# Kernel tuning notes

Measured on AMD Instinct MI355X. Metric: run time of the kernel, lower is better.

## Reference

```python
import jax, jax.numpy as jnp
import numpy as np

ALPHA = 0.2  # LeakyReLU negative slope
NEG_INF = -9e15  # matches torch -9000000000000000.0


def setup_inputs() -> dict:
    key = jax.random.key(0)
    k1, k2, k3, k4, k5, k6 = jax.random.split(key, 6)
    N, F_in, F_out = 4096, 512, 256
    adj = jax.random.randint(k1, (N, N), 0, 2, dtype=jnp.int32)
    h = jax.random.normal(k2, (N, F_in), dtype=jnp.float32)
    # proj: Linear(F_in, F_out)
    W = jax.random.normal(k3, (F_in, F_out), dtype=jnp.float32) * (1.0 / np.sqrt(F_in))
    b = jax.random.normal(k4, (F_out,), dtype=jnp.float32) * 0.01
    # proj_a: Linear(2*F_out, 1) split into the two halves acting on src/dst features
    a1 = jax.random.normal(k5, (F_out,), dtype=jnp.float32) * (1.0 / np.sqrt(2 * F_out))
    a2 = jax.random.normal(k6, (F_out,), dtype=jnp.float32) * (1.0 / np.sqrt(2 * F_out))
    a_b = jnp.zeros((), dtype=jnp.float32)
    return {"adj": adj, "h": h, "W": W, "b": b, "a1": a1, "a2": a2, "a_b": a_b}


def reference(adj, h, W, b, a1, a2, a_b):
    # wh = proj(h): [N, F_out]
    wh = h @ W + b
    # Fused form of the N x N x 2F concat + Linear(2F,1):
    # logits[i, j] = wh[i] . a1 + wh[j] . a2 + a_b
    f_src = wh @ a1  # [N]
    f_dst = wh @ a2  # [N]
    e = jax.nn.leaky_relu(f_src[:, None] + f_dst[None, :] + a_b, negative_slope=ALPHA)
    e = jnp.where(adj > 0, e, NEG_INF)
    att = jax.nn.softmax(e, axis=-1)  # F.softmax legacy dim=1 for 2D
    # dropout: inference mode (no-op) for deterministic reference
    out = att @ wh  # [N, F_out]
    return jax.nn.elu(out)  # concat=True
```

## Files before the change

kernel.cpp:

```cpp
#include <hip/hip_runtime.h>

#define NN   4096
#define FIN  512
#define FOUT 256
#define ALPHA 0.2f

typedef __attribute__((ext_vector_type(8))) short short8;
typedef __attribute__((ext_vector_type(4))) float f32x4;
typedef unsigned short u16;

__device__ __forceinline__ u16 f2bf(float x) {
    union { float f; unsigned u; } v; v.f = x;
    unsigned r = v.u + 0x7FFF + ((v.u >> 16) & 1);
    return (u16)(r >> 16);
}

__global__ __launch_bounds__(256) void k_wt(const float* __restrict__ W,
                                            u16* __restrict__ Wt,
                                            float* __restrict__ fs,
                                            float* __restrict__ fd) {
    __shared__ float s[64 * 65];
    const int t  = threadIdx.x;
    const int g  = (blockIdx.y * gridDim.x + blockIdx.x) * 256 + t;
    if (g < NN) fs[g] = 0.f; else fd[g - NN] = 0.f;
    const int f0 = blockIdx.x * 64;
    const int k0 = blockIdx.y * 64;
    #pragma unroll
    for (int p = 0; p < 4; ++p) {
        int q = t + 256 * p, rr = q >> 4, cc = q & 15;
        float4 w4 = *(const float4*)&W[(size_t)(k0 + rr) * FOUT + f0 + cc * 4];
        s[(cc * 4 + 0) * 65 + rr] = w4.x;
        s[(cc * 4 + 1) * 65 + rr] = w4.y;
        s[(cc * 4 + 2) * 65 + rr] = w4.z;
        s[(cc * 4 + 3) * 65 + rr] = w4.w;
    }
    __syncthreads();
    #pragma unroll
    for (int p = 0; p < 4; ++p) {
        int q = t + 256 * p, f = q >> 4, kg = q & 15;
        ushort4 o;
        o.x = f2bf(s[f * 65 + kg * 4 + 0]);
        o.y = f2bf(s[f * 65 + kg * 4 + 1]);
        o.z = f2bf(s[f * 65 + kg * 4 + 2]);
        o.w = f2bf(s[f * 65 + kg * 4 + 3]);
        *(ushort4*)&Wt[(size_t)(f0 + f) * FIN + k0 + kg * 4] = o;
    }
}

#define HS 520
__global__ __launch_bounds__(256) void k_proj(const float* __restrict__ h,
                                              const u16* __restrict__ Wt,
                                              const float* __restrict__ bias,
                                              const float* __restrict__ a1,
                                              const float* __restrict__ a2,
                                              u16* __restrict__ whT,
                                              float* __restrict__ fs,
                                              float* __restrict__ fd) {
    __shared__ u16 s_h[32 * HS];
    const int t  = threadIdx.x;
    const int f0 = blockIdx.x * 64;
    const int i0 = blockIdx.y * 32;
    #pragma unroll
    for (int p = 0; p < 16; ++p) {
        int q = t + 256 * p, row = q >> 7, c4 = q & 127;
        float4 v = *(const float4*)&h[(size_t)(i0 + row) * FIN + c4 * 4];
        ushort4 o; o.x = f2bf(v.x); o.y = f2bf(v.y); o.z = f2bf(v.z); o.w = f2bf(v.w);
        *(ushort4*)&s_h[row * HS + c4 * 4] = o;
    }
    __syncthreads();
    const int w = t >> 6, l = t & 63, n = l & 15, quad = l >> 4;
    const int hh = w & 1, fh = w >> 1;
    f32x4 acc[2] = {{0.f,0.f,0.f,0.f},{0.f,0.f,0.f,0.f}};
    #pragma unroll
    for (int k0 = 0; k0 < FIN; k0 += 32) {
        short8 a = *(const short8*)&s_h[(hh * 16 + n) * HS + k0 + quad * 8];
        short8 b0 = *(const short8*)&Wt[(size_t)(f0 + fh * 32 + n) * FIN + k0 + quad * 8];
        short8 b1 = *(const short8*)&Wt[(size_t)(f0 + fh * 32 + 16 + n) * FIN + k0 + quad * 8];
        acc[0] = __builtin_amdgcn_mfma_f32_16x16x32_bf16(a, b0, acc[0], 0, 0, 0);
        acc[1] = __builtin_amdgcn_mfma_f32_16x16x32_bf16(a, b1, acc[1], 0, 0, 0);
    }
    const int fb = f0 + fh * 32 + n;
    const float bv0 = bias[fb],  bv1 = bias[fb + 16];
    const float a10 = a1[fb],    a11 = a1[fb + 16];
    const float a20 = a2[fb],    a21 = a2[fb + 16];
    u16* wt_tile = whT + (size_t)(i0 >> 5) * (FOUT * 32);
    float d1[4], d2[4];
    #pragma unroll
    for (int r = 0; r < 4; ++r) {
        const int ic = hh * 16 + quad * 4 + r;
        const float v0 = acc[0][r] + bv0;
        const float v1 = acc[1][r] + bv1;
        wt_tile[fb * 32 + ic]        = f2bf(v0);
        wt_tile[(fb + 16) * 32 + ic] = f2bf(v1);
        d1[r] = v0 * a10 + v1 * a11;
        d2[r] = v0 * a20 + v1 * a21;
    }
    #pragma unroll
    for (int m = 1; m < 16; m <<= 1) {
        #pragma unroll
        for (int r = 0; r < 4; ++r) {
            d1[r] += __shfl_xor(d1[r], m);
            d2[r] += __shfl_xor(d2[r], m);
        }
    }
    if (n == 0) {
        #pragma unroll
        for (int r = 0; r < 4; ++r) {
            const int i = i0 + hh * 16 + quad * 4 + r;
            atomicAdd(&fs[i], d1[r]);
            atomicAdd(&fd[i], d2[r]);
        }
    }
}

__global__ __launch_bounds__(256) void k_exp(const float* __restrict__ fd,
                                             float* __restrict__ Fj,
                                             float* __restrict__ Hj) {
    const int g = blockIdx.x * 256 + threadIdx.x;
    float4 v = ((const float4*)fd)[g];
    float4 F, H;
    F.x = __expf(v.x); F.y = __expf(v.y); F.z = __expf(v.z); F.w = __expf(v.w);
    H.x = __expf(ALPHA * v.x); H.y = __expf(ALPHA * v.y);
    H.z = __expf(ALPHA * v.z); H.w = __expf(ALPHA * v.w);
    ((float4*)Fj)[g] = F;
    ((float4*)Hj)[g] = H;
}

#define BI 32
#define KJ 32
#define CJ 8
__global__ __launch_bounds__(256) void k_attn(const int* __restrict__ adj,
                                              const u16* __restrict__ whT,
                                              const float* __restrict__ fs,
                                              const float* __restrict__ Fj,
                                              const float* __restrict__ Hj,
                                              const float* __restrict__ ab,
                                              float* __restrict__ part,
                                              float* __restrict__ psum) {
    const int t = threadIdx.x;
    const int w = t >> 6, l = t & 63, n = l & 15, quad = l >> 4;
    const int i0 = blockIdx.x * BI;
    const int c  = blockIdx.y;
    const int jbeg = c * (NN / CJ), jend = jbeg + (NN / CJ);
    const int fw  = w * 64;
    const int jq8 = quad * 8;

    const float abv = ab[0];
    const float s0 = fs[i0 + n] + abv;
    const float s1 = fs[i0 + 16 + n] + abv;
    const float E0 = __expf(s0), G0 = __expf(ALPHA * s0), R0 = __expf(-s0);
    const float E1 = __expf(s1), G1 = __expf(ALPHA * s1), R1 = __expf(-s1);

    f32x4 acc[2][4] = {{{0.f,0.f,0.f,0.f},{0.f,0.f,0.f,0.f},{0.f,0.f,0.f,0.f},{0.f,0.f,0.f,0.f}},
                       {{0.f,0.f,0.f,0.f},{0.f,0.f,0.f,0.f},{0.f,0.f,0.f,0.f},{0.f,0.f,0.f,0.f}}};
    float rs0 = 0.f, rs1 = 0.f;

    const size_t ar0 = (size_t)(i0 + n) * NN;
    const size_t ar1 = (size_t)(i0 + 16 + n) * NN;

    int4 c0a = *(const int4*)&adj[ar0 + jbeg + jq8];
    int4 c0b = *(const int4*)&adj[ar0 + jbeg + jq8 + 4];
    int4 c1a = *(const int4*)&adj[ar1 + jbeg + jq8];
    int4 c1b = *(const int4*)&adj[ar1 + jbeg + jq8 + 4];

#define PEL(FV, HV, AV, E, G, R, OO, IDX, RS) do {            \
        float _mi = (FV) >= (R) ? (E) : (G);                  \
        float _mj = (FV) >= (R) ? (FV) : (HV);                \
        float _p  = ((AV) > 0) ? _mi * _mj : 0.f;             \
        OO.e[IDX] = f2bf(_p); RS += _p; } while (0)

    #pragma unroll 2
    for (int j0 = jbeg; j0 < jend; j0 += KJ) {
        const u16* tb = whT + (size_t)(j0 >> 5) * (FOUT * 32) + quad * 8;
        short8 b[4];
        #pragma unroll
        for (int u = 0; u < 4; ++u)
            b[u] = *(const short8*)&tb[(fw + u * 16 + n) * 32];
        float4 Fa = *(const float4*)&Fj[j0 + jq8];
        float4 Fb = *(const float4*)&Fj[j0 + jq8 + 4];
        float4 Ha = *(const float4*)&Hj[j0 + jq8];
        float4 Hb = *(const float4*)&Hj[j0 + jq8 + 4];
        int4 a0a = c0a, a0b = c0b, a1a = c1a, a1b = c1b;
        if (j0 + KJ < jend) {
            c0a = *(const int4*)&adj[ar0 + j0 + KJ + jq8];
            c0b = *(const int4*)&adj[ar0 + j0 + KJ + jq8 + 4];
            c1a = *(const int4*)&adj[ar1 + j0 + KJ + jq8];
            c1b = *(const int4*)&adj[ar1 + j0 + KJ + jq8 + 4];
        }
        union { short8 v; u16 e[8]; } o0, o1;
        PEL(Fa.x, Ha.x, a0a.x, E0, G0, R0, o0, 0, rs0);
        PEL(Fa.y, Ha.y, a0a.y, E0, G0, R0, o0, 1, rs0);
        PEL(Fa.z, Ha.z, a0a.z, E0, G0, R0, o0, 2, rs0);
        PEL(Fa.w, Ha.w, a0a.w, E0, G0, R0, o0, 3, rs0);
        PEL(Fb.x, Hb.x, a0b.x, E0, G0, R0, o0, 4, rs0);
        PEL(Fb.y, Hb.y, a0b.y, E0, G0, R0, o0, 5, rs0);
        PEL(Fb.z, Hb.z, a0b.z, E0, G0, R0, o0, 6, rs0);
        PEL(Fb.w, Hb.w, a0b.w, E0, G0, R0, o0, 7, rs0);
        PEL(Fa.x, Ha.x, a1a.x, E1, G1, R1, o1, 0, rs1);
        PEL(Fa.y, Ha.y, a1a.y, E1, G1, R1, o1, 1, rs1);
        PEL(Fa.z, Ha.z, a1a.z, E1, G1, R1, o1, 2, rs1);
        PEL(Fa.w, Ha.w, a1a.w, E1, G1, R1, o1, 3, rs1);
        PEL(Fb.x, Hb.x, a1b.x, E1, G1, R1, o1, 4, rs1);
        PEL(Fb.y, Hb.y, a1b.y, E1, G1, R1, o1, 5, rs1);
        PEL(Fb.z, Hb.z, a1b.z, E1, G1, R1, o1, 6, rs1);
        PEL(Fb.w, Hb.w, a1b.w, E1, G1, R1, o1, 7, rs1);
        #pragma unroll
        for (int u = 0; u < 4; ++u) {
            acc[0][u] = __builtin_amdgcn_mfma_f32_16x16x32_bf16(o0.v, b[u], acc[0][u], 0, 0, 0);
            acc[1][u] = __builtin_amdgcn_mfma_f32_16x16x32_bf16(o1.v, b[u], acc[1][u], 0, 0, 0);
        }
    }
#undef PEL
    rs0 += __shfl_xor(rs0, 16); rs0 += __shfl_xor(rs0, 32);
    rs1 += __shfl_xor(rs1, 16); rs1 += __shfl_xor(rs1, 32);
    if (w == 0 && quad == 0) {
        psum[(size_t)c * NN + i0 + n]      = rs0;
        psum[(size_t)c * NN + i0 + 16 + n] = rs1;
    }
    float* pc = part + ((size_t)c * NN + i0) * FOUT;
    #pragma unroll
    for (int hf = 0; hf < 2; ++hf)
        #pragma unroll
        for (int u = 0; u < 4; ++u)
            #pragma unroll
            for (int r = 0; r < 4; ++r)
                pc[(size_t)(hf * 16 + quad * 4 + r) * FOUT + fw + u * 16 + n] = acc[hf][u][r];
}

__global__ __launch_bounds__(256) void k_fin(const float* __restrict__ part,
                                             const float* __restrict__ psum,
                                             float* __restrict__ out, int C) {
    const int g = blockIdx.x * 256 + threadIdx.x;
    const int i = g >> 6;
    const size_t s4 = (size_t)NN * FOUT / 4;
    float4 a = ((const float4*)part)[g];
    float s = psum[i];
    for (int c = 1; c < C; ++c) {
        float4 bb = ((const float4*)part)[g + (size_t)c * s4];
        a.x += bb.x; a.y += bb.y; a.z += bb.z; a.w += bb.w;
        s += psum[(size_t)c * NN + i];
    }
    const float inv = 1.0f / s;
    a.x *= inv; a.y *= inv; a.z *= inv; a.w *= inv;
    a.x = a.x > 0.f ? a.x : __expf(a.x) - 1.f;
    a.y = a.y > 0.f ? a.y : __expf(a.y) - 1.f;
    a.z = a.z > 0.f ? a.z : __expf(a.z) - 1.f;
    a.w = a.w > 0.f ? a.w : __expf(a.w) - 1.f;
    ((float4*)out)[g] = a;
}

extern "C" void kernel_launch(void* const* d_in, const int* in_sizes, int n_in,
                              void* d_out, int out_size, void* d_ws, size_t ws_size,
                              hipStream_t stream) {
    const int*   adj = (const int*)  d_in[0];
    const float* h   = (const float*)d_in[1];
    const float* W   = (const float*)d_in[2];
    const float* b   = (const float*)d_in[3];
    const float* a1  = (const float*)d_in[4];
    const float* a2  = (const float*)d_in[5];
    const float* ab  = (const float*)d_in[6];
    float* out = (float*)d_out;

    const int C = CJ;

    float* fs   = (float*)d_ws;
    float* fd   = fs + NN;
    float* Fjv  = fd + NN;
    float* Hjv  = Fjv + NN;
    float* psum = Hjv + NN;
    float* part = psum + (size_t)C * NN;
    u16*   Wt   = (u16*)(part + (size_t)C * NN * FOUT);
    u16*   whT  = Wt + (size_t)FOUT * FIN;

    k_wt  <<<dim3(FOUT / 64, FIN / 64), 256, 0, stream>>>(W, Wt, fs, fd);
    k_proj<<<dim3(FOUT / 64, NN / 32), 256, 0, stream>>>(h, Wt, b, a1, a2, whT, fs, fd);
    k_exp <<<NN / 1024, 256, 0, stream>>>(fd, Fjv, Hjv);
    k_attn<<<dim3(NN / BI, C), 256, 0, stream>>>(adj, whT, fs, Fjv, Hjv, ab, part, psum);
    k_fin <<<(NN * FOUT / 4) / 256, 256, 0, stream>>>(part, psum, out, C);
}
```

Measured before the change: 176.7 us.

## Pack adjacency into bitmask in a pre-pass and use max-form LeakyReLU exp

Adds a kernel that ballots the int32 adjacency matrix into a 1-bit-per-edge mask. The attention kernel then reads compact mask words instead of int4 adjacency loads. Previously the 64MB adjacency was read once per feature-wave (4 waves per block), so it was re-read redundantly; now it is read once in full and the attention kernel reads only 2MB of bits. The per-element LeakyReLU exp is also simplified to fmax(E*F, G*H), which drops the comparison against exp(-s). The cost is an extra kernel launch and a full pass over the adjacency matrix.

Result: faster. 171.0 us (-3.2%).

```diff
diff --git a/kernel.cpp b/kernel.cpp
--- a/kernel.cpp
+++ b/kernel.cpp
@@ -8,6 +8,7 @@
 typedef __attribute__((ext_vector_type(8))) short short8;
 typedef __attribute__((ext_vector_type(4))) float f32x4;
 typedef unsigned short u16;
+typedef unsigned int u32;
 
 __device__ __forceinline__ u16 f2bf(float x) {
     union { float f; unsigned u; } v; v.f = x;
@@ -44,6 +45,24 @@
         o.z = f2bf(s[f * 65 + kg * 4 + 2]);
         o.w = f2bf(s[f * 65 + kg * 4 + 3]);
         *(ushort4*)&Wt[(size_t)(f0 + f) * FIN + k0 + kg * 4] = o;
+    }
+}
+
+__global__ __launch_bounds__(256) void k_bits(const int* __restrict__ adj,
+                                              unsigned long long* __restrict__ bits) {
+    const int t = threadIdx.x, l = t & 63;
+    const int row = blockIdx.x * 4 + (t >> 6);
+    const size_t base = (size_t)row * NN;
+    #pragma unroll 4
+    for (int o = 0; o < 16; ++o) {
+        unsigned long long b0 = __ballot(adj[base + (o * 4 + 0) * 64 + l] > 0);
+        unsigned long long b1 = __ballot(adj[base + (o * 4 + 1) * 64 + l] > 0);
+        unsigned long long b2 = __ballot(adj[base + (o * 4 + 2) * 64 + l] > 0);
+        unsigned long long b3 = __ballot(adj[base + (o * 4 + 3) * 64 + l] > 0);
+        if (l == 0) {
+            unsigned long long* d = bits + (size_t)row * 64 + o * 4;
+            d[0] = b0; d[1] = b1; d[2] = b2; d[3] = b3;
+        }
     }
 }
 
@@ -127,9 +146,8 @@
 }
 
 #define BI 32
-#define KJ 32
 #define CJ 8
-__global__ __launch_bounds__(256) void k_attn(const int* __restrict__ adj,
+__global__ __launch_bounds__(256) void k_attn(const u32* __restrict__ bits,
                                               const u16* __restrict__ whT,
                                               const float* __restrict__ fs,
                                               const float* __restrict__ Fj,
@@ -148,66 +166,65 @@
     const float abv = ab[0];
     const float s0 = fs[i0 + n] + abv;
     const float s1 = fs[i0 + 16 + n] + abv;
-    const float E0 = __expf(s0), G0 = __expf(ALPHA * s0), R0 = __expf(-s0);
-    const float E1 = __expf(s1), G1 = __expf(ALPHA * s1), R1 = __expf(-s1);
+    const float E0 = __expf(s0), G0 = __expf(ALPHA * s0);
+    const float E1 = __expf(s1), G1 = __expf(ALPHA * s1);
 
     f32x4 acc[2][4] = {{{0.f,0.f,0.f,0.f},{0.f,0.f,0.f,0.f},{0.f,0.f,0.f,0.f},{0.f,0.f,0.f,0.f}},
                        {{0.f,0.f,0.f,0.f},{0.f,0.f,0.f,0.f},{0.f,0.f,0.f,0.f},{0.f,0.f,0.f,0.f}}};
     float rs0 = 0.f, rs1 = 0.f;
 
-    const size_t ar0 = (size_t)(i0 + n) * NN;
-    const size_t ar1 = (size_t)(i0 + 16 + n) * NN;
-
-    int4 c0a = *(const int4*)&adj[ar0 + jbeg + jq8];
-    int4 c0b = *(const int4*)&adj[ar0 + jbeg + jq8 + 4];
-    int4 c1a = *(const int4*)&adj[ar1 + jbeg + jq8];
-    int4 c1b = *(const int4*)&adj[ar1 + jbeg + jq8 + 4];
-
-#define PEL(FV, HV, AV, E, G, R, OO, IDX, RS) do {            \
-        float _mi = (FV) >= (R) ? (E) : (G);                  \
-        float _mj = (FV) >= (R) ? (FV) : (HV);                \
-        float _p  = ((AV) > 0) ? _mi * _mj : 0.f;             \
+    const u32* B0 = bits + (size_t)(i0 + n) * 128;
+    const u32* B1 = bits + (size_t)(i0 + 16 + n) * 128;
+    uint4 m0 = *(const uint4*)&B0[jbeg >> 5];
+    uint4 m1 = *(const uint4*)&B1[jbeg >> 5];
+
+#define PEL(FV, HV, BW, K, E, G, OO, IDX, RS) do {            \
+        float _p = fmaxf((E) * (FV), (G) * (HV));             \
+        _p = ((BW) & (1u << (K))) ? _p : 0.f;                 \
         OO.e[IDX] = f2bf(_p); RS += _p; } while (0)
 
-    #pragma unroll 2
-    for (int j0 = jbeg; j0 < jend; j0 += KJ) {
-        const u16* tb = whT + (size_t)(j0 >> 5) * (FOUT * 32) + quad * 8;
-        short8 b[4];
-        #pragma unroll
-        for (int u = 0; u < 4; ++u)
-            b[u] = *(const short8*)&tb[(fw + u * 16 + n) * 32];
-        float4 Fa = *(const float4*)&Fj[j0 + jq8];
-        float4 Fb = *(const float4*)&Fj[j0 + jq8 + 4];
-        float4 Ha = *(const float4*)&Hj[j0 + jq8];
-        float4 Hb = *(const float4*)&Hj[j0 + jq8 + 4];
-        int4 a0a = c0a, a0b = c0b, a1a = c1a, a1b = c1b;
-        if (j0 + KJ < jend) {
-            c0a = *(const int4*)&adj[ar0 + j0 + KJ + jq8];
-            c0b = *(const int4*)&adj[ar0 + j0 + KJ + jq8 + 4];
-            c1a = *(const int4*)&adj[ar1 + j0 + KJ + jq8];
-            c1b = *(const int4*)&adj[ar1 + j0 + KJ + jq8 + 4];
-        }
-        union { short8 v; u16 e[8]; } o0, o1;
-        PEL(Fa.x, Ha.x, a0a.x, E0, G0, R0, o0, 0, rs0);
-        PEL(Fa.y, Ha.y, a0a.y, E0, G0, R0, o0, 1, rs0);
-        PEL(Fa.z, Ha.z, a0a.z, E0, G0, R0, o0, 2, rs0);
-        PEL(Fa.w, Ha.w, a0a.w, E0, G0, R0, o0, 3, rs0);
-        PEL(Fb.x, Hb.x, a0b.x, E0, G0, R0, o0, 4, rs0);
-        PEL(Fb.y, Hb.y, a0b.y, E0, G0, R0, o0, 5, rs0);
-        PEL(Fb.z, Hb.z, a0b.z, E0, G0, R0, o0, 6, rs0);
-        PEL(Fb.w, Hb.w, a0b.w, E0, G0, R0, o0, 7, rs0);
-        PEL(Fa.x, Ha.x, a1a.x, E1, G1, R1, o1, 0, rs1);
-        PEL(Fa.y, Ha.y, a1a.y, E1, G1, R1, o1, 1, rs1);
-        PEL(Fa.z, Ha.z, a1a.z, E1, G1, R1, o1, 2, rs1);
-        PEL(Fa.w, Ha.w, a1a.w, E1, G1, R1, o1, 3, rs1);
-        PEL(Fb.x, Hb.x, a1b.x, E1, G1, R1, o1, 4, rs1);
-        PEL(Fb.y, Hb.y, a1b.y, E1, G1, R1, o1, 5, rs1);
-        PEL(Fb.z, Hb.z, a1b.z, E1, G1, R1, o1, 6, rs1);
-        PEL(Fb.w, Hb.w, a1b.w, E1, G1, R1, o1, 7, rs1);
-        #pragma unroll
-        for (int u = 0; u < 4; ++u) {
-            acc[0][u] = __builtin_amdgcn_mfma_f32_16x16x32_bf16(o0.v, b[u], acc[0][u], 0, 0, 0);
-            acc[1][u] = __builtin_amdgcn_mfma_f32_16x16x32_bf16(o1.v, b[u], acc[1][u], 0, 0, 0);
+    for (int jb = jbeg; jb < jend; jb += 128) {
+        const uint4 cm0 = m0, cm1 = m1;
+        if (jb + 128 < jend) {
+            m0 = *(const uint4*)&B0[(jb + 128) >> 5];
+            m1 = *(const uint4*)&B1[(jb + 128) >> 5];
+        }
+        #pragma unroll
+        for (int s = 0; s < 4; ++s) {
+            const int j0 = jb + s * 32;
+            const u32 bw0 = (s == 0 ? cm0.x : s == 1 ? cm0.y : s == 2 ? cm0.z : cm0.w) >> jq8;
+            const u32 bw1 = (s == 0 ? cm1.x : s == 1 ? cm1.y : s == 2 ? cm1.z : cm1.w) >> jq8;
+            const u16* tb = whT + (size_t)(j0 >> 5) * (FOUT * 32) + quad * 8;
+            short8 b[4];
+            #pragma unroll
+            for (int u = 0; u < 4; ++u)
+                b[u] = *(const short8*)&tb[(fw + u * 16 + n) * 32];
+            float4 Fa = *(const float4*)&Fj[j0 + jq8];
+            float4 Fb = *(const float4*)&Fj[j0 + jq8 + 4];
+            float4 Ha = *(const float4*)&Hj[j0 + jq8];
+            float4 Hb = *(const float4*)&Hj[j0 + jq8 + 4];
+            union { short8 v; u16 e[8]; } o0, o1;
+            PEL(Fa.x, Ha.x, bw0, 0, E0, G0, o0, 0, rs0);
+            PEL(Fa.y, Ha.y, bw0, 1, E0, G0, o0, 1, rs0);
+            PEL(Fa.z, Ha.z, bw0, 2, E0, G0, o0, 2, rs0);
+            PEL(Fa.w, Ha.w, bw0, 3, E0, G0, o0, 3, rs0);
+            PEL(Fb.x, Hb.x, bw0, 4, E0, G0, o0, 4, rs0);
+            PEL(Fb.y, Hb.y, bw0, 5, E0, G0, o0, 5, rs0);
+            PEL(Fb.z, Hb.z, bw0, 6, E0, G0, o0, 6, rs0);
+            PEL(Fb.w, Hb.w, bw0, 7, E0, G0, o0, 7, rs0);
+            PEL(Fa.x, Ha.x, bw1, 0, E1, G1, o1, 0, rs1);
+            PEL(Fa.y, Ha.y, bw1, 1, E1, G1, o1, 1, rs1);
+            PEL(Fa.z, Ha.z, bw1, 2, E1, G1, o1, 2, rs1);
+            PEL(Fa.w, Ha.w, bw1, 3, E1, G1, o1, 3, rs1);
+            PEL(Fb.x, Hb.x, bw1, 4, E1, G1, o1, 4, rs1);
+            PEL(Fb.y, Hb.y, bw1, 5, E1, G1, o1, 5, rs1);
+            PEL(Fb.z, Hb.z, bw1, 6, E1, G1, o1, 6, rs1);
+            PEL(Fb.w, Hb.w, bw1, 7, E1, G1, o1, 7, rs1);
+            #pragma unroll
+            for (int u = 0; u < 4; ++u) {
+                acc[0][u] = __builtin_amdgcn_mfma_f32_16x16x32_bf16(o0.v, b[u], acc[0][u], 0, 0, 0);
+                acc[1][u] = __builtin_amdgcn_mfma_f32_16x16x32_bf16(o1.v, b[u], acc[1][u], 0, 0, 0);
+            }
         }
     }
 #undef PEL
@@ -271,10 +288,12 @@
     float* part = psum + (size_t)C * NN;
     u16*   Wt   = (u16*)(part + (size_t)C * NN * FOUT);
     u16*   whT  = Wt + (size_t)FOUT * FIN;
+    unsigned long long* bits = (unsigned long long*)(whT + (size_t)NN * FOUT);
 
     k_wt  <<<dim3(FOUT / 64, FIN / 64), 256, 0, stream>>>(W, Wt, fs, fd);
+    k_bits<<<NN / 4, 256, 0, stream>>>(adj, bits);
     k_proj<<<dim3(FOUT / 64, NN / 32), 256, 0, stream>>>(h, Wt, b, a1, a2, whT, fs, fd);
     k_exp <<<NN / 1024, 256, 0, stream>>>(fd, Fjv, Hjv);
-    k_attn<<<dim3(NN / BI, C), 256, 0, stream>>>(adj, whT, fs, Fjv, Hjv, ab, part, psum);
+    k_attn<<<dim3(NN / BI, C), 256, 0, stream>>>((const u32*)bits, whT, fs, Fjv, Hjv, ab, part, psum);
     k_fin <<<(NN * FOUT / 4) / 256, 256, 0, stream>>>(part, psum, out, C);
 }
```
